# Kernel optimization log

Measured on AMD Instinct MI355X. Metric: run time of the kernel, lower is better.

The kernel has to match this reference:

```python
import jax, jax.numpy as jnp
import numpy as np

# Hyperparameters matching GyroLoss(__init__)
W = 1.0e6        # w
MIN_N = 4        # min_N -> min_train_freq = 16
MAX_N = 5        # max_N -> max_train_freq = 32
DT = 0.01        # dt (100 Hz IMU)
HUBER = 0.005    # huber delta
N0 = 5           # warm-up steps dropped from the residual
MIN_TRAIN_FREQ = 2 ** MIN_N


def _skew(v):
    # v: [M,3] -> [M,3,3] skew-symmetric matrices
    x, y, z = v[..., 0], v[..., 1], v[..., 2]
    o = jnp.zeros_like(x)
    return jnp.stack([
        jnp.stack([o, -z,  y], -1),
        jnp.stack([z,  o, -x], -1),
        jnp.stack([-y, x,  o], -1),
    ], -2)


def so3_exp(phi):
    # Rodrigues formula, phi: [M,3] -> R: [M,3,3]
    sq = jnp.sum(phi * phi, -1, keepdims=True)          # [M,1]
    angle = jnp.sqrt(jnp.maximum(sq, 1e-16))
    small = sq < 1e-12
    a = jnp.where(small, 1.0, angle)
    s = jnp.where(small, 1.0 - sq / 6.0, jnp.sin(a) / a)
    c = jnp.where(small, 0.5 - sq / 24.0, (1.0 - jnp.cos(a)) / (a * a))
    K = _skew(phi)
    I = jnp.eye(3, dtype=phi.dtype)
    return I + s[..., None] * K + c[..., None] * jnp.matmul(K, K)


def so3_log(R):
    # R: [M,3,3] -> phi: [M,3]
    tr = R[..., 0, 0] + R[..., 1, 1] + R[..., 2, 2]
    cos = jnp.clip(0.5 * (tr - 1.0), -1.0 + 1e-7, 1.0 - 1e-7)
    angle = jnp.arccos(cos)
    s = angle / (2.0 * jnp.sin(angle))
    vee = jnp.stack([
        R[..., 2, 1] - R[..., 1, 2],
        R[..., 0, 2] - R[..., 2, 0],
        R[..., 1, 0] - R[..., 0, 1],
    ], -1)
    return s[..., None] * vee


def _bmtm(a, b):
    # batched a^T @ b for [M,3,3]
    return jnp.einsum('nij,nik->njk', a, b)


def _f_huber(rs):
    # SmoothL1Loss (beta=1, mean reduction) on rs/HUBER vs zeros, scaled by w*huber^2
    z = rs / HUBER
    az = jnp.abs(z)
    l = jnp.mean(jnp.where(az < 1.0, 0.5 * z * z, az - 0.5))
    return W * l * HUBER ** 2


def setup_inputs() -> dict:
    key = jax.random.key(0)
    k1, k2, k3 = jax.random.split(key, 3)
    N, T = 64, 32768  # T divisible by 2**MAX_N
    xs = jax.random.normal(k1, (N, T, 3), dtype=jnp.float32)
    dp = jax.random.normal(k2, (1, 3), dtype=jnp.float32)  # unused by forward
    hat_xs = jax.random.normal(k3, (N, T, 3), dtype=jnp.float32)
    return {"xs": xs, "dp": dp, "hat_xs": hat_xs}


def reference(xs, dp, hat_xs):
    N = xs.shape[0]
    # ground-truth increments at min_train_freq stride -> rotations
    xs_r = so3_exp(xs[:, ::MIN_TRAIN_FREQ].reshape(-1, 3))       # [N*T/16,3,3]
    # predicted gyro -> per-step rotation increments
    Om = so3_exp((DT * hat_xs).reshape(-1, 3))                    # [N*T,3,3]
    # tree reduction: compose adjacent rotations min_N times
    for _ in range(MIN_N):
        Om = jnp.matmul(Om[::2], Om[1::2])
    rs = so3_log(_bmtm(Om, xs_r)).reshape(N, -1, 3)[:, N0:]
    loss = _f_huber(rs)
    for k in range(MIN_N, MAX_N):
        Om = jnp.matmul(Om[::2], Om[1::2])
        xs_r = jnp.matmul(xs_r[::2], xs_r[1::2])
        rs = so3_log(_bmtm(Om, xs_r)).reshape(N, -1, 3)[:, N0:]
        loss = loss + _f_huber(rs) / 2.0 ** (k - MIN_N + 1)
    return loss
```

## Files before the change

### kernel.cpp

```cpp
#include <hip/hip_runtime.h>
#include <math.h>

#define NSEQ 64
#define TLEN 32768
#define G16_PER_SEQ 2048
#define NG16 (NSEQ * G16_PER_SEQ)
#define STEPS_PER_THREAD 4
#define NTHREADS (NG16 * 4)
#define BLOCK 256
#define NBLOCKS (NTHREADS / BLOCK)
#define N0 5
#define DT 0.01f
#define HUBER_INV 200.0f

__device__ __constant__ float C16 = 25.0f / (64.0f * 2043.0f * 3.0f);
__device__ __constant__ float C32 = 12.5f / (64.0f * 1019.0f * 3.0f);

__device__ __forceinline__ void mat_mul3(const float* A, const float* B, float* C) {
#pragma unroll
    for (int i = 0; i < 3; ++i) {
#pragma unroll
        for (int j = 0; j < 3; ++j) {
            C[3 * i + j] = A[3 * i + 0] * B[0 + j]
                         + A[3 * i + 1] * B[3 + j]
                         + A[3 * i + 2] * B[6 + j];
        }
    }
}

__device__ __forceinline__ void so3_exp_dev(float x, float y, float z, float* R) {
    float sq = x * x + y * y + z * z;
    float angle = sqrtf(fmaxf(sq, 1e-16f));
    bool small = sq < 1e-12f;
    float a = small ? 1.0f : angle;
    float sn, cs;
    __sincosf(a, &sn, &cs);
    float s = small ? (1.0f - sq * (1.0f / 6.0f)) : (sn / a);
    float c = small ? (0.5f - sq * (1.0f / 24.0f)) : ((1.0f - cs) / (a * a));
    float cxx = c * x * x, cyy = c * y * y, czz = c * z * z;
    float cxy = c * x * y, cxz = c * x * z, cyz = c * y * z;
    float sx = s * x, sy = s * y, sz = s * z;
    R[0] = 1.0f - cyy - czz; R[1] = cxy - sz;          R[2] = cxz + sy;
    R[3] = cxy + sz;         R[4] = 1.0f - cxx - czz;  R[5] = cyz - sx;
    R[6] = cxz - sy;         R[7] = cyz + sx;          R[8] = 1.0f - cxx - cyy;
}

__device__ __forceinline__ float huber3_bmtm_log(const float* Om, const float* Xr) {
    float M[9];
#pragma unroll
    for (int j = 0; j < 3; ++j) {
#pragma unroll
        for (int k = 0; k < 3; ++k) {
            M[3 * j + k] = Om[0 + j] * Xr[0 + k]
                         + Om[3 + j] * Xr[3 + k]
                         + Om[6 + j] * Xr[6 + k];
        }
    }
    float tr = M[0] + M[4] + M[8];
    float cosv = 0.5f * (tr - 1.0f);
    cosv = fminf(fmaxf(cosv, -1.0f + 1e-7f), 1.0f - 1e-7f);
    float angle = acosf(cosv);
    float sn = sqrtf(fmaxf(1.0f - cosv * cosv, 0.0f));
    float sfac = angle / (2.0f * sn);
    float v0 = sfac * (M[7] - M[5]);
    float v1 = sfac * (M[2] - M[6]);
    float v2 = sfac * (M[3] - M[1]);
    float acc = 0.0f;
#pragma unroll
    for (int t = 0; t < 3; ++t) {
        float zz = (t == 0 ? v0 : (t == 1 ? v1 : v2)) * HUBER_INV;
        float az = fabsf(zz);
        acc += (az < 1.0f) ? 0.5f * zz * zz : az - 0.5f;
    }
    return acc;
}

__device__ __forceinline__ void ordered_combine(float* A, int mask, bool upper) {
    float L[9], R[9];
#pragma unroll
    for (int t = 0; t < 9; ++t) {
        float b = __shfl_xor(A[t], mask);
        L[t] = upper ? b : A[t];
        R[t] = upper ? A[t] : b;
    }
    float C[9];
    mat_mul3(L, R, C);
#pragma unroll
    for (int t = 0; t < 9; ++t) A[t] = C[t];
}

__global__ __launch_bounds__(256, 4) void gyro_loss_kernel(const float* __restrict__ xs,
                                                           const float* __restrict__ hat_xs,
                                                           float* __restrict__ partials) {
    __shared__ float lds[BLOCK * 12];
    const int tid = threadIdx.x;
    const int gt = blockIdx.x * BLOCK + tid;

    const float4* gp = reinterpret_cast<const float4*>(hat_xs) + (size_t)blockIdx.x * (BLOCK * 3);
    float4* lp = reinterpret_cast<float4*>(lds);
#pragma unroll
    for (int q = 0; q < 3; ++q) lp[q * BLOCK + tid] = gp[q * BLOCK + tid];
    __syncthreads();

    const float* h = &lds[12 * tid];
    float Ra[9], Rb[9], P[9], Q[9], Om[9];
    so3_exp_dev(DT * h[0], DT * h[1], DT * h[2], Ra);
    so3_exp_dev(DT * h[3], DT * h[4], DT * h[5], Rb);
    mat_mul3(Ra, Rb, P);
    so3_exp_dev(DT * h[6], DT * h[7], DT * h[8], Ra);
    so3_exp_dev(DT * h[9], DT * h[10], DT * h[11], Rb);
    mat_mul3(Ra, Rb, Q);
    mat_mul3(P, Q, Om);

    ordered_combine(Om, 1, (tid & 1) != 0);
    ordered_combine(Om, 2, (tid & 2) != 0);
    const int g = gt >> 2;

    float4 xv = *(reinterpret_cast<const float4*>(xs) + (size_t)g * 12);
    float Xr[9];
    so3_exp_dev(xv.x, xv.y, xv.z, Xr);

    float partial = 0.0f;
    if ((tid & 3) == 0 && (g & (G16_PER_SEQ - 1)) >= N0)
        partial = C16 * huber3_bmtm_log(Om, Xr);

    ordered_combine(Om, 4, (tid & 4) != 0);
    ordered_combine(Xr, 4, (tid & 4) != 0);
    if ((tid & 7) == 0 && ((g >> 1) & (G16_PER_SEQ / 2 - 1)) >= N0)
        partial += C32 * huber3_bmtm_log(Om, Xr);

#pragma unroll
    for (int off = 32; off > 0; off >>= 1) partial += __shfl_down(partial, off);
    __shared__ float wsum[4];
    const int lane = tid & 63;
    const int wid = tid >> 6;
    if (lane == 0) wsum[wid] = partial;
    __syncthreads();
    if (tid == 0) partials[blockIdx.x] = wsum[0] + wsum[1] + wsum[2] + wsum[3];
}

__global__ __launch_bounds__(256) void finish_kernel(const float* __restrict__ partials,
                                                     float* __restrict__ out) {
    const int tid = threadIdx.x;
    float s = 0.0f;
#pragma unroll
    for (int q = 0; q < NBLOCKS / 256; ++q) s += partials[q * 256 + tid];
#pragma unroll
    for (int off = 32; off > 0; off >>= 1) s += __shfl_down(s, off);
    __shared__ float wsum[4];
    if ((tid & 63) == 0) wsum[tid >> 6] = s;
    __syncthreads();
    if (tid == 0) out[0] = wsum[0] + wsum[1] + wsum[2] + wsum[3];
}

extern "C" void kernel_launch(void* const* d_in, const int* in_sizes, int n_in,
                              void* d_out, int out_size, void* d_ws, size_t ws_size,
                              hipStream_t stream) {
    const float* xs     = (const float*)d_in[0];
    const float* hat_xs = (const float*)d_in[2];
    float* out = (float*)d_out;
    float* partials = (float*)d_ws;

    gyro_loss_kernel<<<NBLOCKS, BLOCK, 0, stream>>>(xs, hat_xs, partials);
    finish_kernel<<<1, 256, 0, stream>>>(partials, out);
}
```

Before: 96.43 us.

## Use Taylor so3_exp, direct loads, split huber lanes, fuse final reduction via atomics

Replaces sincos-based exponential of the scaled gyro increments with a truncated Taylor series, loads hat_xs straight into registers instead of staging through LDS, assigns the 16- and 32-stride log/huber evaluations to different lanes to reduce divergence, and replaces the second reduction kernel with per-block atomic adds plus a last-block counter. It aims to cut ALU work, a barrier, and a kernel launch. The series assumes small rotation angles, and atomic float accumulation makes the summation order nondeterministic; a memset is added per call.

```diff
diff --git a/kernel.cpp b/kernel.cpp
--- a/kernel.cpp
+++ b/kernel.cpp
@@ -5,7 +5,6 @@
 #define TLEN 32768
 #define G16_PER_SEQ 2048
 #define NG16 (NSEQ * G16_PER_SEQ)
-#define STEPS_PER_THREAD 4
 #define NTHREADS (NG16 * 4)
 #define BLOCK 256
 #define NBLOCKS (NTHREADS / BLOCK)
@@ -28,6 +27,22 @@
     }
 }
 
+__device__ __forceinline__ void rodrigues(float x, float y, float z, float s, float c, float* R) {
+    float cxx = c * x * x, cyy = c * y * y, czz = c * z * z;
+    float cxy = c * x * y, cxz = c * x * z, cyz = c * y * z;
+    float sx = s * x, sy = s * y, sz = s * z;
+    R[0] = 1.0f - cyy - czz; R[1] = cxy - sz;          R[2] = cxz + sy;
+    R[3] = cxy + sz;         R[4] = 1.0f - cxx - czz;  R[5] = cyz - sx;
+    R[6] = cxz - sy;         R[7] = cyz + sx;          R[8] = 1.0f - cxx - cyy;
+}
+
+__device__ __forceinline__ void so3_exp_small(float x, float y, float z, float* R) {
+    float sq = x * x + y * y + z * z;
+    float s = 1.0f - (sq * (1.0f / 6.0f)) * (1.0f - sq * (1.0f / 20.0f));
+    float c = 0.5f - (sq * (1.0f / 24.0f)) * (1.0f - sq * (1.0f / 30.0f));
+    rodrigues(x, y, z, s, c, R);
+}
+
 __device__ __forceinline__ void so3_exp_dev(float x, float y, float z, float* R) {
     float sq = x * x + y * y + z * z;
     float angle = sqrtf(fmaxf(sq, 1e-16f));
@@ -37,12 +52,7 @@
     __sincosf(a, &sn, &cs);
     float s = small ? (1.0f - sq * (1.0f / 6.0f)) : (sn / a);
     float c = small ? (0.5f - sq * (1.0f / 24.0f)) : ((1.0f - cs) / (a * a));
-    float cxx = c * x * x, cyy = c * y * y, czz = c * z * z;
-    float cxy = c * x * y, cxz = c * x * z, cyz = c * y * z;
-    float sx = s * x, sy = s * y, sz = s * z;
-    R[0] = 1.0f - cyy - czz; R[1] = cxy - sz;          R[2] = cxz + sy;
-    R[3] = cxy + sz;         R[4] = 1.0f - cxx - czz;  R[5] = cyz - sx;
-    R[6] = cxz - sy;         R[7] = cyz + sx;          R[8] = 1.0f - cxx - cyy;
+    rodrigues(x, y, z, s, c, R);
 }
 
 __device__ __forceinline__ float huber3_bmtm_log(const float* Om, const float* Xr) {
@@ -91,24 +101,21 @@
 
 __global__ __launch_bounds__(256, 4) void gyro_loss_kernel(const float* __restrict__ xs,
                                                            const float* __restrict__ hat_xs,
-                                                           float* __restrict__ partials) {
-    __shared__ float lds[BLOCK * 12];
+                                                           float* __restrict__ acc,
+                                                           unsigned int* __restrict__ ctr,
+                                                           float* __restrict__ out) {
     const int tid = threadIdx.x;
     const int gt = blockIdx.x * BLOCK + tid;
 
-    const float4* gp = reinterpret_cast<const float4*>(hat_xs) + (size_t)blockIdx.x * (BLOCK * 3);
-    float4* lp = reinterpret_cast<float4*>(lds);
-#pragma unroll
-    for (int q = 0; q < 3; ++q) lp[q * BLOCK + tid] = gp[q * BLOCK + tid];
-    __syncthreads();
+    const float4* hp = reinterpret_cast<const float4*>(hat_xs) + (size_t)gt * 3;
+    float4 h0 = hp[0], h1 = hp[1], h2 = hp[2];
 
-    const float* h = &lds[12 * tid];
     float Ra[9], Rb[9], P[9], Q[9], Om[9];
-    so3_exp_dev(DT * h[0], DT * h[1], DT * h[2], Ra);
-    so3_exp_dev(DT * h[3], DT * h[4], DT * h[5], Rb);
+    so3_exp_small(DT * h0.x, DT * h0.y, DT * h0.z, Ra);
+    so3_exp_small(DT * h0.w, DT * h1.x, DT * h1.y, Rb);
     mat_mul3(Ra, Rb, P);
-    so3_exp_dev(DT * h[6], DT * h[7], DT * h[8], Ra);
-    so3_exp_dev(DT * h[9], DT * h[10], DT * h[11], Rb);
+    so3_exp_small(DT * h1.z, DT * h1.w, DT * h2.x, Ra);
+    so3_exp_small(DT * h2.y, DT * h2.z, DT * h2.w, Rb);
     mat_mul3(Ra, Rb, Q);
     mat_mul3(P, Q, Om);
 
@@ -120,37 +127,42 @@
     float Xr[9];
     so3_exp_dev(xv.x, xv.y, xv.z, Xr);
 
-    float partial = 0.0f;
-    if ((tid & 3) == 0 && (g & (G16_PER_SEQ - 1)) >= N0)
-        partial = C16 * huber3_bmtm_log(Om, Xr);
-
+    float Om16[9], Xr16[9];
+#pragma unroll
+    for (int t = 0; t < 9; ++t) { Om16[t] = Om[t]; Xr16[t] = Xr[t]; }
     ordered_combine(Om, 4, (tid & 4) != 0);
     ordered_combine(Xr, 4, (tid & 4) != 0);
-    if ((tid & 7) == 0 && ((g >> 1) & (G16_PER_SEQ / 2 - 1)) >= N0)
-        partial += C32 * huber3_bmtm_log(Om, Xr);
+
+    bool do16 = ((tid & 3) == 1) && ((g & (G16_PER_SEQ - 1)) >= N0);
+    bool do32 = ((tid & 7) == 0) && (((g >> 1) & (G16_PER_SEQ / 2 - 1)) >= N0);
+    float partial = 0.0f;
+    if (do16 || do32) {
+        float A[9], B[9];
+#pragma unroll
+        for (int t = 0; t < 9; ++t) {
+            A[t] = do32 ? Om[t] : Om16[t];
+            B[t] = do32 ? Xr[t] : Xr16[t];
+        }
+        float w = do32 ? C32 : C16;
+        partial = w * huber3_bmtm_log(A, B);
+    }
 
 #pragma unroll
     for (int off = 32; off > 0; off >>= 1) partial += __shfl_down(partial, off);
     __shared__ float wsum[4];
-    const int lane = tid & 63;
-    const int wid = tid >> 6;
-    if (lane == 0) wsum[wid] = partial;
+    if ((tid & 63) == 0) wsum[tid >> 6] = partial;
     __syncthreads();
-    if (tid == 0) partials[blockIdx.x] = wsum[0] + wsum[1] + wsum[2] + wsum[3];
-}
 
-__global__ __launch_bounds__(256) void finish_kernel(const float* __restrict__ partials,
-                                                     float* __restrict__ out) {
-    const int tid = threadIdx.x;
-    float s = 0.0f;
-#pragma unroll
-    for (int q = 0; q < NBLOCKS / 256; ++q) s += partials[q * 256 + tid];
-#pragma unroll
-    for (int off = 32; off > 0; off >>= 1) s += __shfl_down(s, off);
-    __shared__ float wsum[4];
-    if ((tid & 63) == 0) wsum[tid >> 6] = s;
-    __syncthreads();
-    if (tid == 0) out[0] = wsum[0] + wsum[1] + wsum[2] + wsum[3];
+    if (tid == 0) {
+        float bsum = wsum[0] + wsum[1] + wsum[2] + wsum[3];
+        atomicAdd(acc, bsum);
+        __threadfence();
+        unsigned int old = atomicAdd(ctr, 1u);
+        if (old == NBLOCKS - 1) {
+            float total = atomicAdd(acc, 0.0f);
+            out[0] = total;
+        }
+    }
 }
 
 extern "C" void kernel_launch(void* const* d_in, const int* in_sizes, int n_in,
@@ -159,8 +171,10 @@
     const float* xs     = (const float*)d_in[0];
     const float* hat_xs = (const float*)d_in[2];
     float* out = (float*)d_out;
-    float* partials = (float*)d_ws;
 
-    gyro_loss_kernel<<<NBLOCKS, BLOCK, 0, stream>>>(xs, hat_xs, partials);
-    finish_kernel<<<1, 256, 0, stream>>>(partials, out);
+    float* acc        = (float*)d_ws;
+    unsigned int* ctr = (unsigned int*)d_ws + 1;
+
+    hipMemsetAsync(d_ws, 0, 8, stream);
+    gyro_loss_kernel<<<NBLOCKS, BLOCK, 0, stream>>>(xs, hat_xs, acc, ctr, out);
 }
```

After: 143.3 us. 48.6% more time.
